# Optimization experiments

Hardware: AMD Instinct MI355X
Metric: run time of the kernel (lower is better)

Reference implementation:

```python
import jax, jax.numpy as jnp
import numpy as np

H = 512; EMB = 300; TAGE = 20; TRE = 20
VOCAB = 50000; NTAGS = 50; NTRANS = 100; NCONST = 80
B = 128; S = 256; T = 512; R = S // 2


def _lstm_scan(x, Wih, Whh, b):
    # x: [N, L, D] -> hidden states [N, L, H]; torch gate order i, f, g, o
    N = x.shape[0]; Hh = Whh.shape[1]
    xg = jnp.einsum('nld,gd->nlg', x, Wih) + b  # precompute input projections
    def step(carry, xg_t):
        h, c = carry
        g = xg_t + h @ Whh.T
        i, f, gg, o = jnp.split(g, 4, axis=-1)
        c = jax.nn.sigmoid(f) * c + jax.nn.sigmoid(i) * jnp.tanh(gg)
        h = jax.nn.sigmoid(o) * jnp.tanh(c)
        return (h, c), h
    h0 = jnp.zeros((N, Hh), x.dtype)
    _, hs = jax.lax.scan(step, (h0, h0), jnp.swapaxes(xg, 0, 1))
    return jnp.swapaxes(hs, 0, 1)


def setup_inputs() -> dict:
    key = jax.random.key(0)
    ks = iter(jax.random.split(key, 40))
    def p(shape, scale):
        return jax.random.normal(next(ks), shape, jnp.float32) * jnp.float32(scale)
    def lstm_p(din):
        s = 1.0 / np.sqrt(H)
        return p((4 * H, din), s), p((4 * H, H), s), p((4 * H,), s)
    inp = {}
    inp['word_idx'] = jax.random.randint(next(ks), (B, S), 0, VOCAB)
    inp['tag_idx'] = jax.random.randint(next(ks), (B, S), 0, NTAGS)
    inp['transition_idx'] = jax.random.randint(next(ks), (B, T), 0, NTRANS)
    inp['label_idx'] = jax.random.randint(next(ks), (B, R), 0, NCONST)
    inp['emb'] = p((VOCAB, EMB), 1.0)
    inp['tag_emb'] = p((NTAGS, TAGE), 1.0)
    inp['tr_emb'] = p((NTRANS, TRE), 1.0)
    inp['const_emb'] = p((NCONST, H), 1.0)
    inp['word_Wih'], inp['word_Whh'], inp['word_b'] = lstm_p(EMB + TAGE)
    inp['tr_Wih'], inp['tr_Whh'], inp['tr_b'] = lstm_p(TRE)
    inp['con_Wih'], inp['con_Whh'], inp['con_b'] = lstm_p(H)
    inp['fwd_Wih'], inp['fwd_Whh'], inp['fwd_b'] = lstm_p(H)
    inp['bwd_Wih'], inp['bwd_Whh'], inp['bwd_b'] = lstm_p(H)
    inp['w2c_W'] = p((H, H), 1.0 / np.sqrt(H)); inp['w2c_b'] = jnp.zeros((H,), jnp.float32)
    inp['red_W'] = p((H, 2 * H), 1.0 / np.sqrt(2 * H)); inp['red_b'] = jnp.zeros((H,), jnp.float32)
    inp['out_W'] = p((NTRANS, 3 * H), 1.0 / np.sqrt(3 * H)); inp['out_b'] = jnp.zeros((NTRANS,), jnp.float32)
    return inp


def reference(word_idx, tag_idx, transition_idx, label_idx, emb, tag_emb, tr_emb, const_emb, word_Wih, word_Whh, word_b, tr_Wih, tr_Whh, tr_b, con_Wih, con_Whh, con_b, fwd_Wih, fwd_Whh, fwd_b, bwd_Wih, bwd_Whh, bwd_b, w2c_W, w2c_b, red_W, red_b, out_W, out_b):
    Bn, Sn = word_idx.shape
    Rn = label_idx.shape[1]
    # initial_word_queue: word emb + tag emb -> word LSTM
    word_in = jnp.concatenate([emb[word_idx], tag_emb[tag_idx]], axis=-1)  # [B,S,EMB+TAGE]
    word_h = _lstm_scan(word_in, word_Wih, word_Whh, word_b)              # [B,S,H]
    # transform_word_to_constituent
    c0 = word_h @ w2c_W.T + w2c_b                                         # [B,S,H]
    # build_constituent: label emb + 2 children through fwd/bwd reduce LSTMs
    lab = const_emb[label_idx]                                            # [B,R,H]
    ch0 = c0[:, 0::2][:, :Rn]; ch1 = c0[:, 1::2][:, :Rn]
    fwd_seq = jnp.stack([lab, ch0, ch1], axis=2).reshape(Bn * Rn, 3, -1)
    bwd_seq = jnp.stack([lab, ch1, ch0], axis=2).reshape(Bn * Rn, 3, -1)
    fh = _lstm_scan(fwd_seq, fwd_Wih, fwd_Whh, fwd_b)[:, -1]
    bh = _lstm_scan(bwd_seq, bwd_Wih, bwd_Whh, bwd_b)[:, -1]
    red = jnp.tanh(jnp.concatenate([fh, bh], -1) @ red_W.T + red_b).reshape(Bn, Rn, -1)
    # push_constituent: constituent LSTMCell scan over built constituents
    const_h = _lstm_scan(red, con_Wih, con_Whh, con_b)[:, -1]             # [B,H]
    # push_transition: transition LSTMCell scan
    tr_h = _lstm_scan(tr_emb[transition_idx], tr_Wih, tr_Whh, tr_b)[:, -1]  # [B,H]
    # forward(): W over concat(word_hx, transition_hx, constituent_hx)
    hx = jnp.concatenate([word_h[:, -1], tr_h, const_h], axis=-1)         # [B,3H]
    return hx @ out_W.T + out_b                                           # [B,NTRANS]
```

## Files before the change

### kernel.cpp

```cpp
#include <hip/hip_runtime.h>

typedef unsigned short u16;
typedef unsigned int u32;
typedef unsigned long long u64;
typedef __attribute__((ext_vector_type(8))) short short8;
typedef __attribute__((ext_vector_type(4))) float f32x4;

namespace {
constexpr int kS  = 256;
constexpr int kT  = 512;
constexpr int kNT = 100;
constexpr int LDST = 40;
}

__device__ __forceinline__ float bf(u16 v){ return __uint_as_float(((u32)v)<<16); }
__device__ __forceinline__ u16 f2bf(float f){
  u32 u = __float_as_uint(f);
  return (u16)((u + 0x7fffu + ((u>>16)&1u)) >> 16);
}
__device__ __forceinline__ float sigm(float x){ return 1.f/(1.f+__expf(-x)); }
__device__ __forceinline__ float tanha(float x){ return 2.f/(1.f+__expf(-2.f*x)) - 1.f; }
__device__ __forceinline__ float wred(float v){
  #pragma unroll
  for (int off=32; off>0; off>>=1) v += __shfl_xor(v, off, 64);
  return v;
}

__device__ __forceinline__ u64 ld_sys_u64(const void* p){
  return __hip_atomic_load((const u64*)p, __ATOMIC_RELAXED, __HIP_MEMORY_SCOPE_SYSTEM);
}
__device__ __forceinline__ void st_sys_u32(void* p, u32 v){
  __hip_atomic_store((u32*)p, v, __ATOMIC_RELAXED, __HIP_MEMORY_SCOPE_SYSTEM);
}
__device__ __forceinline__ u32 ld_sys_u32(const void* p){
  return __hip_atomic_load((const u32*)p, __ATOMIC_RELAXED, __HIP_MEMORY_SCOPE_SYSTEM);
}

__global__ void k_zero(u32* p, int n){
  const int i = blockIdx.x*256 + threadIdx.x;
  if (i < n) p[i] = 0;
}

struct SeqJob {
  u16* hseq; u16* hb0; u16* hb1;
  const u16* xg; const int* idx;
  float* c_io;
  const u16* Bw;
  u32* flags;
  int s_begin, s_end, mode, c_store;
};

__global__ __launch_bounds__(256,1) void k_seq2(SeqJob jA, SeqJob jB)
{
  __shared__ u16 Bs[32*520];
  __shared__ float c_lds[128*9];
  __shared__ float sc[4*4*16*20];
  const SeqJob j = (blockIdx.x < 64) ? jA : jB;
  const int gb = blockIdx.x & 63;
  const int tid = threadIdx.x;
  const int ln = tid & 63, w = tid >> 6, wm = w * 32;
  const int fr = ln & 15, koff = (ln >> 4) * 8;
  const int n0 = gb * 32, jh0 = gb * 8;

  for (int e = tid; e < 2048; e += 256) {
    const int cl = e >> 6, kb = (e & 63) * 8;
    *(uint4*)&Bs[cl*520 + kb] = *(const uint4*)&j.Bw[(size_t)(n0+cl)*512 + kb];
  }
  for (int e = tid; e < 1024; e += 256) {
    const int m = e >> 3, jj = e & 7;
    c_lds[m*9 + jj] = j.c_io[(size_t)m*512 + jh0 + jj];
  }
  __syncthreads();

  const size_t aoff0 = (size_t)(wm + fr)*512 + koff;
  const size_t aoff1 = (size_t)(wm + 16 + fr)*512 + koff;
  const int cr = (ln>>4)*4, cc = ln&15;
  const int trow = ln>>2, pp = ln&3, ntp = pp>>1, cp = pp&1;
  const f32x4 z4 = {0.f,0.f,0.f,0.f};

  for (int s = j.s_begin; s < j.s_end; ++s) {
    const u16* Ab; u16* hout;
    if (j.mode == 0) { Ab = j.hseq + (size_t)(s-1)*65536; hout = j.hseq + (size_t)s*65536; }
    else { Ab = ((s-1)&1) ? j.hb1 : j.hb0; hout = (s&1) ? j.hb1 : j.hb0; }
    const u16* xgs = (j.mode == 0) ? (j.xg + (size_t)s*262144) : j.xg;

    u64 aq0[16][2], aq1[16][2];
    #pragma unroll
    for (int kt = 0; kt < 16; ++kt) {
      aq0[kt][0] = ld_sys_u64(&Ab[aoff0 + kt*32]);
      aq0[kt][1] = ld_sys_u64(&Ab[aoff0 + kt*32 + 4]);
      aq1[kt][0] = ld_sys_u64(&Ab[aoff1 + kt*32]);
      aq1[kt][1] = ld_sys_u64(&Ab[aoff1 + kt*32 + 4]);
    }
    f32x4 acc[2][2] = {{z4,z4},{z4,z4}};
    #pragma unroll
    for (int kt = 0; kt < 16; ++kt) {
      union { u64 q[2]; short8 v; } ua, ub;
      ua.q[0] = aq0[kt][0]; ua.q[1] = aq0[kt][1];
      ub.q[0] = aq1[kt][0]; ub.q[1] = aq1[kt][1];
      const short8 b0 = *(const short8*)&Bs[fr*520 + kt*32 + koff];
      const short8 b1 = *(const short8*)&Bs[(16+fr)*520 + kt*32 + koff];
      acc[0][0] = __builtin_amdgcn_mfma_f32_16x16x32_bf16(ua.v, b0, acc[0][0], 0,0,0);
      acc[0][1] = __builtin_amdgcn_mfma_f32_16x16x32_bf16(ua.v, b1, acc[0][1], 0,0,0);
      acc[1][0] = __builtin_amdgcn_mfma_f32_16x16x32_bf16(ub.v, b0, acc[1][0], 0,0,0);
      acc[1][1] = __builtin_amdgcn_mfma_f32_16x16x32_bf16(ub.v, b1, acc[1][1], 0,0,0);
    }

    #pragma unroll
    for (int mt=0; mt<2; ++mt)
      #pragma unroll
      for (int nt=0; nt<2; ++nt) {
        float* scb = &sc[(size_t)(w*4 + mt*2 + nt)*320];
        #pragma unroll
        for (int ri=0; ri<4; ++ri) scb[(cr+ri)*20 + cc] = acc[mt][nt][ri];
      }
    #pragma unroll
    for (int mt=0; mt<2; ++mt) {
      const int m = wm + mt*16 + trow;
      const float* scb = &sc[(size_t)(w*4+mt*2+ntp)*320 + trow*20 + cp*8];
      const float4 zlo = *(const float4*)&scb[0];
      const float4 zhi = *(const float4*)&scb[4];
      long xr;
      if (j.mode == 0) xr = m;
      else if (j.mode == 1) xr = j.idx[(size_t)m*512 + s];
      else xr = (long)m*128 + s;
      union { uint4 u4; u16 h[8]; } xq;
      xq.u4 = *(const uint4*)&xgs[(size_t)xr*2048 + n0 + ntp*16 + cp*8];
      const int cj = m*9 + ntp*4 + cp*2;
      float h0, h1;
      {
        const float i_ = sigm(zlo.x + bf(xq.h[0]));
        const float f_ = sigm(zlo.y + bf(xq.h[1]));
        const float g_ = tanha(zlo.z + bf(xq.h[2]));
        const float o_ = sigm(zlo.w + bf(xq.h[3]));
        const float cn = f_*c_lds[cj] + i_*g_;
        c_lds[cj] = cn;
        h0 = o_*tanha(cn);
      }
      {
        const float i_ = sigm(zhi.x + bf(xq.h[4]));
        const float f_ = sigm(zhi.y + bf(xq.h[5]));
        const float g_ = tanha(zhi.z + bf(xq.h[6]));
        const float o_ = sigm(zhi.w + bf(xq.h[7]));
        const float cn = f_*c_lds[cj+1] + i_*g_;
        c_lds[cj+1] = cn;
        h1 = o_*tanha(cn);
      }
      const u32 pk = (u32)f2bf(h0) | ((u32)f2bf(h1) << 16);
      st_sys_u32(&hout[(size_t)m*512 + jh0 + ntp*4 + cp*2], pk);
    }

    __builtin_amdgcn_s_waitcnt(0);
    __syncthreads();
    if (tid == 0)
      st_sys_u32(j.flags + (gb << 5), (u32)s);
    if (s + 1 < j.s_end) {
      if (tid < 64) {
        while (true) {
          u32 f = ld_sys_u32(j.flags + (tid << 5));
          if (__all((int)(f >= (u32)s))) break;
          __builtin_amdgcn_s_sleep(2);
        }
      }
      __syncthreads();
    }
  }
  if (j.c_store) {
    __syncthreads();
    for (int e = tid; e < 1024; e += 256) {
      const int m = e >> 3, jj = e & 7;
      j.c_io[(size_t)m*512 + jh0 + jj] = c_lds[m*9 + jj];
    }
  }
}

__device__ __forceinline__ void gemm_core(
    const u16* __restrict__ A, const u16* __restrict__ B, int K,
    int m0, int n0, u16* As, u16* Bs, f32x4 acc[4][4], int tid)
{
  const int lane = tid & 63;
  const int w = tid >> 6;
  const int wm = (w & 1) * 64, wn = (w >> 1) * 64;
  const int fr = lane & 15;
  const int fq = (lane >> 4) * 8;
  for (int k0 = 0; k0 < K; k0 += 32) {
    __syncthreads();
    #pragma unroll
    for (int it = 0; it < 2; ++it) {
      const int l = tid + it * 256;
      const int r = l >> 2, kq = (l & 3) * 8;
      *(uint4*)&As[r * LDST + kq] = *(const uint4*)&A[(size_t)(m0 + r) * K + k0 + kq];
      *(uint4*)&Bs[r * LDST + kq] = *(const uint4*)&B[(size_t)(n0 + r) * K + k0 + kq];
    }
    __syncthreads();
    short8 af[4], bfr[4];
    #pragma unroll
    for (int t = 0; t < 4; ++t) {
      af[t]  = *(const short8*)&As[(wm + t * 16 + fr) * LDST + fq];
      bfr[t] = *(const short8*)&Bs[(wn + t * 16 + fr) * LDST + fq];
    }
    #pragma unroll
    for (int mt = 0; mt < 4; ++mt)
      #pragma unroll
      for (int nt = 0; nt < 4; ++nt)
        acc[mt][nt] = __builtin_amdgcn_mfma_f32_16x16x32_bf16(af[mt], bfr[nt], acc[mt][nt], 0, 0, 0);
  }
}

__global__ __launch_bounds__(256) void k_gemm(
    const u16* __restrict__ A, const u16* __restrict__ B, u16* __restrict__ C,
    const float* __restrict__ bias, int K, int N, int tanh_flag)
{
  __shared__ u16 As[128 * LDST];
  __shared__ u16 Bs[128 * LDST];
  const int tid = threadIdx.x;
  const int m0 = blockIdx.x * 128, n0 = blockIdx.y * 128;
  f32x4 acc[4][4];
  const f32x4 z4 = {0.f, 0.f, 0.f, 0.f};
  #pragma unroll
  for (int mt = 0; mt < 4; ++mt)
    #pragma unroll
    for (int nt = 0; nt < 4; ++nt) acc[mt][nt] = z4;

  gemm_core(A, B, K, m0, n0, As, Bs, acc, tid);

  const int lane = tid & 63;
  const int w = tid >> 6;
  const int wm = (w & 1) * 64, wn = (w >> 1) * 64;
  const int cr = (lane >> 4) * 4, cc = lane & 15;
  #pragma unroll
  for (int mt = 0; mt < 4; ++mt)
    #pragma unroll
    for (int nt = 0; nt < 4; ++nt)
      #pragma unroll
      for (int ri = 0; ri < 4; ++ri) {
        const int row = m0 + wm + mt * 16 + cr + ri;
        const int col = n0 + wn + nt * 16 + cc;
        float v = acc[mt][nt][ri];
        if (bias) v += bias[col];
        if (tanh_flag) v = tanha(v);
        C[(size_t)row * N + col] = f2bf(v);
      }
}

__global__ __launch_bounds__(256) void k_lstm_cat(
    const u16* __restrict__ H, const u16* __restrict__ X,
    const u16* __restrict__ B, const float* __restrict__ bias,
    const int* __restrict__ idx, int cmode, int p0, int first,
    float* __restrict__ c_st, u16* __restrict__ h_out, int h_stride, int h_coloff)
{
  __shared__ u16 As[128 * LDST];
  __shared__ u16 Bs[128 * LDST];
  __shared__ float zb[64 * 128];
  const int tid = threadIdx.x;
  const int m0 = blockIdx.x * 128, n0 = blockIdx.y * 128;
  const int lane = tid & 63;
  const int w = tid >> 6;
  const int wm = (w & 1) * 64, wn = (w >> 1) * 64;
  const int fr = lane & 15, fq = (lane >> 4) * 8;
  f32x4 acc[4][4];
  const f32x4 z4 = {0.f, 0.f, 0.f, 0.f};
  #pragma unroll
  for (int mt = 0; mt < 4; ++mt)
    #pragma unroll
    for (int nt = 0; nt < 4; ++nt) acc[mt][nt] = z4;

  for (int k0 = first ? 512 : 0; k0 < 1024; k0 += 32) {
    __syncthreads();
    #pragma unroll
    for (int it = 0; it < 2; ++it) {
      const int l = tid + it * 256;
      const int r = l >> 2, kq = (l & 3) * 8;
      const int m = m0 + r;
      const u16* src;
      if (k0 < 512) {
        src = H + (size_t)m * 512 + k0 + kq;
      } else {
        long xr;
        if (cmode == 1)      xr = (long)(2 * (m & 127) + p0) * 128 + (m >> 7);
        else if (cmode == 2) xr = (long)idx[m];
        else                 xr = (long)m * 128 + p0;
        src = X + (size_t)xr * 512 + (k0 - 512) + kq;
      }
      *(uint4*)&As[r * LDST + kq] = *(const uint4*)src;
      *(uint4*)&Bs[r * LDST + kq] = *(const uint4*)&B[(size_t)(n0 + r) * 1024 + k0 + kq];
    }
    __syncthreads();
    short8 af[4], bfr[4];
    #pragma unroll
    for (int t = 0; t < 4; ++t) {
      af[t]  = *(const short8*)&As[(wm + t * 16 + fr) * LDST + fq];
      bfr[t] = *(const short8*)&Bs[(wn + t * 16 + fr) * LDST + fq];
    }
    #pragma unroll
    for (int mt = 0; mt < 4; ++mt)
      #pragma unroll
      for (int nt = 0; nt < 4; ++nt)
        acc[mt][nt] = __builtin_amdgcn_mfma_f32_16x16x32_bf16(af[mt], bfr[nt], acc[mt][nt], 0, 0, 0);
  }

  const int cr = (lane >> 4) * 4, cc = lane & 15;
  #pragma unroll
  for (int half = 0; half < 2; ++half) {
    __syncthreads();
    if (wm == half * 64) {
      #pragma unroll
      for (int mt = 0; mt < 4; ++mt)
        #pragma unroll
        for (int nt = 0; nt < 4; ++nt)
          #pragma unroll
          for (int ri = 0; ri < 4; ++ri)
            zb[(mt * 16 + cr + ri) * 128 + wn + nt * 16 + cc] = acc[mt][nt][ri];
    }
    __syncthreads();
    for (int c = tid; c < 2048; c += 256) {
      const int rl = c >> 5;
      const int q  = c & 31;
      const int m  = m0 + half * 64 + rl;
      const int jh = (n0 >> 2) + q;
      const float4 bv = *(const float4*)&bias[n0 + q * 4];
      const float4 zv = *(const float4*)&zb[rl * 128 + q * 4];
      const float i_ = sigm(zv.x + bv.x);
      const float f_ = sigm(zv.y + bv.y);
      const float g_ = tanha(zv.z + bv.z);
      const float o_ = sigm(zv.w + bv.w);
      const size_t ci = (size_t)m * 512 + jh;
      const float cold = first ? 0.f : c_st[ci];
      const float cn = f_ * cold + i_ * g_;
      c_st[ci] = cn;
      h_out[(size_t)m * h_stride + h_coloff + jh] = f2bf(o_ * tanha(cn));
    }
  }
}

__global__ __launch_bounds__(256) void k_gate0(
    const u16* __restrict__ xg, int xg_mode, int p0,
    const int* __restrict__ idx, int istride,
    float* __restrict__ c_st, u16* __restrict__ h_out, int h_stride, int h_coloff, int M)
{
  const int id = blockIdx.x * 256 + threadIdx.x;
  if (id >= M * 512) return;
  const int m = id >> 9, jh = id & 511;
  long xr;
  if (xg_mode == 0) xr = (long)m * p0;
  else              xr = (long)idx[(size_t)m * istride];
  const ushort4 xq = *(const ushort4*)&xg[(size_t)xr * 2048 + jh * 4];
  const float i_ = sigm(bf(xq.x));
  const float g_ = tanha(bf(xq.z));
  const float o_ = sigm(bf(xq.w));
  const float cn = i_ * g_;
  c_st[(size_t)m * 512 + jh] = cn;
  h_out[(size_t)m * h_stride + h_coloff + jh] = f2bf(o_ * tanha(cn));
}

__global__ void k_perm_w(const float* __restrict__ in, u16* __restrict__ out,
                         int Ksrc, int Kfill, int Ktot, int coff)
{
  const int rp = blockIdx.x;
  const int g = rp & 3, jh = rp >> 2;
  const float* src = in + (size_t)(g * 512 + jh) * Ksrc;
  for (int k = threadIdx.x; k < Kfill; k += 256)
    out[(size_t)rp * Ktot + coff + k] = f2bf(k < Ksrc ? src[k] : 0.f);
}
__global__ void k_perm_b(const float* __restrict__ in, float* __restrict__ out)
{
  const int rp = blockIdx.x * 256 + threadIdx.x;
  out[rp] = in[(rp & 3) * 512 + (rp >> 2)];
}
__global__ void k_cvt(const float* __restrict__ in, u16* __restrict__ out, int n)
{
  const int i = blockIdx.x * 256 + threadIdx.x;
  if (i < n) out[i] = f2bf(in[i]);
}
__global__ void k_pad2d(const float* __restrict__ in, u16* __restrict__ out,
                        int Rin, int Kin, int Kout)
{
  const int r = blockIdx.x;
  for (int k = threadIdx.x; k < Kout; k += 256)
    out[(size_t)r * Kout + k] = f2bf((r < Rin && k < Kin) ? in[(size_t)r * Kin + k] : 0.f);
}
__global__ void k_gather_word(const int* __restrict__ widx, const int* __restrict__ tidx,
                              const float* __restrict__ emb, const float* __restrict__ temb,
                              u16* __restrict__ Aw)
{
  const int row = blockIdx.x;
  const int s = row >> 7, b = row & 127;
  const int wi = widx[b * kS + s];
  const int ti = tidx[b * kS + s];
  for (int t = threadIdx.x; t < 320; t += 256)
    Aw[(size_t)row * 320 + t] = f2bf(t < 300 ? emb[(size_t)wi * 300 + t] : temb[ti * 20 + t - 300]);
}

__global__ __launch_bounds__(256) void k_out(
    const u16* __restrict__ wh, const u16* __restrict__ trh, const u16* __restrict__ conh,
    const float* __restrict__ W, const float* __restrict__ bias, float* __restrict__ out)
{
  const int wid = blockIdx.x * 4 + (threadIdx.x >> 6);
  const int lane = threadIdx.x & 63;
  const int b = wid / kNT;
  const int t = wid - b * kNT;
  const u16* s0 = wh + (size_t)b * 512;
  const u16* s1 = trh + (size_t)b * 512;
  const u16* s2 = conh + (size_t)b * 512;
  const float* wr = W + (size_t)t * 1536;
  float acc = 0.f;
  #pragma unroll
  for (int i = 0; i < 8; ++i) acc += bf(s0[i * 64 + lane]) * wr[i * 64 + lane];
  #pragma unroll
  for (int i = 0; i < 8; ++i) acc += bf(s1[i * 64 + lane]) * wr[512 + i * 64 + lane];
  #pragma unroll
  for (int i = 0; i < 8; ++i) acc += bf(s2[i * 64 + lane]) * wr[1024 + i * 64 + lane];
  acc = wred(acc);
  if (lane == 0) out[(size_t)b * kNT + t] = acc + bias[t];
}

extern "C" void kernel_launch(void* const* d_in, const int* in_sizes, int n_in,
                              void* d_out, int out_size, void* d_ws, size_t ws_size,
                              hipStream_t stream)
{
  (void)in_sizes; (void)n_in; (void)out_size; (void)ws_size;
  const int* word_idx = (const int*)d_in[0];
  const int* tag_idx  = (const int*)d_in[1];
  const int* tr_idx   = (const int*)d_in[2];
  const int* lab_idx  = (const int*)d_in[3];
  const float* emb       = (const float*)d_in[4];
  const float* tag_emb   = (const float*)d_in[5];
  const float* tr_emb    = (const float*)d_in[6];
  const float* const_emb = (const float*)d_in[7];
  const float* word_Wih = (const float*)d_in[8];
  const float* word_Whh = (const float*)d_in[9];
  const float* word_b   = (const float*)d_in[10];
  const float* tr_Wih = (const float*)d_in[11];
  const float* tr_Whh = (const float*)d_in[12];
  const float* tr_b   = (const float*)d_in[13];
  const float* con_Wih = (const float*)d_in[14];
  const float* con_Whh = (const float*)d_in[15];
  const float* con_b   = (const float*)d_in[16];
  const float* fwd_Wih = (const float*)d_in[17];
  const float* fwd_Whh = (const float*)d_in[18];
  const float* fwd_b   = (const float*)d_in[19];
  const float* bwd_Wih = (const float*)d_in[20];
  const float* bwd_Whh = (const float*)d_in[21];
  const float* bwd_b   = (const float*)d_in[22];
  const float* w2c_W = (const float*)d_in[23];
  const float* w2c_b = (const float*)d_in[24];
  const float* red_W = (const float*)d_in[25];
  const float* red_b = (const float*)d_in[26];
  const float* out_W = (const float*)d_in[27];
  const float* out_b = (const float*)d_in[28];

  char* p = (char*)d_ws;
  auto alloc = [&](size_t bytes)->void* {
    void* r = (void*)p; p += (bytes + 255) & ~(size_t)255; return r;
  };
  u16* word_h = (u16*)alloc((size_t)32768*512*2);
  char* R     = (char*)alloc((size_t)155189248);
  u16* A_word = (u16*)(R);
  u16* XGword = (u16*)(R + 20971520);
  u16* c0     = (u16*)(R);
  u16* h1     = (u16*)(R + 33554432);
  u16* h2     = (u16*)(R + 50331648);
  float* c_big= (float*)(R + 67108864);
  u16* fb     = (u16*)(R + 100663296);
  u16* red    = (u16*)(R + 134217728);
  u16* XG_con = (u16*)(R);
  u16* wWih = (u16*)alloc((size_t)2048*320*2);
  u16* wWhh = (u16*)alloc((size_t)2048*512*2);
  u16* tWih = (u16*)alloc((size_t)2048*32*2);
  u16* tWhh = (u16*)alloc((size_t)2048*512*2);
  u16* cWihp = (u16*)alloc((size_t)2048*512*2);
  u16* cWhhp = (u16*)alloc((size_t)2048*512*2);
  u16* fWcat = (u16*)alloc((size_t)2048*1024*2);
  u16* bWcat = (u16*)alloc((size_t)2048*1024*2);
  u16* fWih  = (u16*)alloc((size_t)2048*512*2);
  u16* bWih  = (u16*)alloc((size_t)2048*512*2);
  u16* w2cWb = (u16*)alloc((size_t)512*512*2);
  u16* redWb = (u16*)alloc((size_t)512*1024*2);
  u16* A80   = (u16*)alloc((size_t)128*512*2);
  u16* Atr   = (u16*)alloc((size_t)128*32*2);
  u16* tbltr = (u16*)alloc((size_t)128*2048*2);
  u16* tbl0  = (u16*)alloc((size_t)128*2048*2);
  float* b_word = (float*)alloc(2048*4);
  float* b_tr   = (float*)alloc(2048*4);
  float* b_con  = (float*)alloc(2048*4);
  float* b_fwd  = (float*)alloc(2048*4);
  float* b_bwd  = (float*)alloc(2048*4);
  float* c_word = (float*)alloc((size_t)128*512*4);
  float* c_tr   = (float*)alloc((size_t)128*512*4);
  float* c_con  = (float*)alloc((size_t)128*512*4);
  u16* trh1 = (u16*)alloc((size_t)128*512*2);
  u16* trh2 = (u16*)alloc((size_t)128*512*2);
  u16* ch1  = (u16*)alloc((size_t)128*512*2);
  u16* ch2  = (u16*)alloc((size_t)128*512*2);
  u32* flags = (u32*)alloc((size_t)4*64*32*4);

  k_zero<<<32,256,0,stream>>>(flags, 4*64*32);

  k_perm_w<<<2048,256,0,stream>>>(word_Wih, wWih, 320, 320, 320, 0);
  k_perm_w<<<2048,256,0,stream>>>(word_Whh, wWhh, 512, 512, 512, 0);
  k_perm_w<<<2048,256,0,stream>>>(tr_Wih,   tWih, 20,  32,  32,  0);
  k_perm_w<<<2048,256,0,stream>>>(tr_Whh,   tWhh, 512, 512, 512, 0);
  k_perm_w<<<2048,256,0,stream>>>(con_Wih,  cWihp, 512, 512, 512, 0);
  k_perm_w<<<2048,256,0,stream>>>(con_Whh,  cWhhp, 512, 512, 512, 0);
  k_perm_w<<<2048,256,0,stream>>>(fwd_Whh,  fWcat, 512, 512, 1024, 0);
  k_perm_w<<<2048,256,0,stream>>>(fwd_Wih,  fWcat, 512, 512, 1024, 512);
  k_perm_w<<<2048,256,0,stream>>>(bwd_Whh,  bWcat, 512, 512, 1024, 0);
  k_perm_w<<<2048,256,0,stream>>>(bwd_Wih,  bWcat, 512, 512, 1024, 512);
  k_perm_w<<<2048,256,0,stream>>>(fwd_Wih,  fWih, 512, 512, 512, 0);
  k_perm_w<<<2048,256,0,stream>>>(bwd_Wih,  bWih, 512, 512, 512, 0);
  k_perm_b<<<8,256,0,stream>>>(word_b, b_word);
  k_perm_b<<<8,256,0,stream>>>(tr_b,   b_tr);
  k_perm_b<<<8,256,0,stream>>>(con_b,  b_con);
  k_perm_b<<<8,256,0,stream>>>(fwd_b,  b_fwd);
  k_perm_b<<<8,256,0,stream>>>(bwd_b,  b_bwd);
  k_cvt<<<1024,256,0,stream>>>(w2c_W, w2cWb, 512*512);
  k_cvt<<<2048,256,0,stream>>>(red_W, redWb, 512*1024);
  k_pad2d<<<128,256,0,stream>>>(const_emb, A80, 80, 512, 512);
  k_pad2d<<<128,256,0,stream>>>(tr_emb,    Atr, 100, 20, 32);
  k_gather_word<<<32768,256,0,stream>>>(word_idx, tag_idx, emb, tag_emb, A_word);

  k_gemm<<<dim3(256,16),256,0,stream>>>(A_word, wWih, XGword, b_word, 320, 2048, 0);
  k_gemm<<<dim3(1,16),256,0,stream>>>(Atr, tWih, tbltr, b_tr, 32, 2048, 0);

  k_gate0<<<256,256,0,stream>>>(XGword, 0, 1, nullptr, 0, c_word, word_h, 512, 0, 128);
  k_gate0<<<256,256,0,stream>>>(tbltr, 2, 0, tr_idx, 512, c_tr, trh1, 512, 0, 128);

  SeqJob jw{ word_h, nullptr, nullptr, XGword, nullptr, c_word, wWhh, flags + 0*2048, 1, 256, 0, 0 };
  SeqJob jt1{ nullptr, trh1, trh2, tbltr, tr_idx, c_tr, tWhh, flags + 1*2048, 1, 256, 1, 1 };
  k_seq2<<<128,256,0,stream>>>(jw, jt1);

  k_gemm<<<dim3(256,4),256,0,stream>>>(word_h, w2cWb, c0, w2c_b, 512, 512, 0);

  k_gemm<<<dim3(1,16),256,0,stream>>>(A80, fWih, tbl0, b_fwd, 512, 2048, 0);
  k_gate0<<<32768,256,0,stream>>>(tbl0, 2, 0, lab_idx, 1, c_big, h1, 512, 0, 16384);
  k_lstm_cat<<<dim3(128,16),256,0,stream>>>(h1, c0, fWcat, b_fwd, nullptr, 1, 0, 0, c_big, h2, 512, 0);
  k_lstm_cat<<<dim3(128,16),256,0,stream>>>(h2, c0, fWcat, b_fwd, nullptr, 1, 1, 0, c_big, fb, 1024, 0);
  k_gemm<<<dim3(1,16),256,0,stream>>>(A80, bWih, tbl0, b_bwd, 512, 2048, 0);
  k_gate0<<<32768,256,0,stream>>>(tbl0, 2, 0, lab_idx, 1, c_big, h1, 512, 0, 16384);
  k_lstm_cat<<<dim3(128,16),256,0,stream>>>(h1, c0, bWcat, b_bwd, nullptr, 1, 1, 0, c_big, h2, 512, 0);
  k_lstm_cat<<<dim3(128,16),256,0,stream>>>(h2, c0, bWcat, b_bwd, nullptr, 1, 0, 0, c_big, fb, 1024, 512);

  k_gemm<<<dim3(128,4),256,0,stream>>>(fb, redWb, red, red_b, 1024, 512, 1);

  k_gemm<<<dim3(128,16),256,0,stream>>>(red, cWihp, XG_con, b_con, 512, 2048, 0);

  k_gate0<<<256,256,0,stream>>>(XG_con, 0, 128, nullptr, 0, c_con, ch1, 512, 0, 128);

  SeqJob jc{ nullptr, ch1, ch2, XG_con, nullptr, c_con, cWhhp, flags + 2*2048, 1, 128, 2, 0 };
  SeqJob jt2{ nullptr, trh1, trh2, tbltr, tr_idx, c_tr, tWhh, flags + 3*2048, 256, 512, 1, 0 };
  k_seq2<<<128,256,0,stream>>>(jc, jt2);

  k_out<<<3200,256,0,stream>>>(word_h + (size_t)255*128*512, trh2, ch2,
                               out_W, out_b, (float*)d_out);
}
```

Before: 6.398 ms.

## Use ring-buffered hidden-state sequences so recurrent loads are plain vector loads

```diff
diff --git a/kernel.cpp b/kernel.cpp
--- a/kernel.cpp
+++ b/kernel.cpp
@@ -26,9 +26,6 @@
   return v;
 }
 
-__device__ __forceinline__ u64 ld_sys_u64(const void* p){
-  return __hip_atomic_load((const u64*)p, __ATOMIC_RELAXED, __HIP_MEMORY_SCOPE_SYSTEM);
-}
 __device__ __forceinline__ void st_sys_u32(void* p, u32 v){
   __hip_atomic_store((u32*)p, v, __ATOMIC_RELAXED, __HIP_MEMORY_SCOPE_SYSTEM);
 }
@@ -42,7 +39,7 @@
 }
 
 struct SeqJob {
-  u16* hseq; u16* hb0; u16* hb1;
+  u16* hseq;
   const u16* xg; const int* idx;
   float* c_io;
   const u16* Bw;
@@ -79,25 +76,35 @@
   const f32x4 z4 = {0.f,0.f,0.f,0.f};
 
   for (int s = j.s_begin; s < j.s_end; ++s) {
-    const u16* Ab; u16* hout;
-    if (j.mode == 0) { Ab = j.hseq + (size_t)(s-1)*65536; hout = j.hseq + (size_t)s*65536; }
-    else { Ab = ((s-1)&1) ? j.hb1 : j.hb0; hout = (s&1) ? j.hb1 : j.hb0; }
+    const u16* Ab = j.hseq + (size_t)((s-1)&255)*65536;
+    u16* hout     = j.hseq + (size_t)(s&255)*65536;
     const u16* xgs = (j.mode == 0) ? (j.xg + (size_t)s*262144) : j.xg;
 
-    u64 aq0[16][2], aq1[16][2];
+    int xrow[2];
+    #pragma unroll
+    for (int mt = 0; mt < 2; ++mt) {
+      const int m = wm + mt*16 + trow;
+      if (j.mode == 1)      xrow[mt] = j.idx[(size_t)m*512 + s];
+      else if (j.mode == 0) xrow[mt] = m;
+      else                  xrow[mt] = m*128 + s;
+    }
+
+    uint4 aq0[16], aq1[16];
     #pragma unroll
     for (int kt = 0; kt < 16; ++kt) {
-      aq0[kt][0] = ld_sys_u64(&Ab[aoff0 + kt*32]);
-      aq0[kt][1] = ld_sys_u64(&Ab[aoff0 + kt*32 + 4]);
-      aq1[kt][0] = ld_sys_u64(&Ab[aoff1 + kt*32]);
-      aq1[kt][1] = ld_sys_u64(&Ab[aoff1 + kt*32 + 4]);
-    }
+      aq0[kt] = *(const uint4*)&Ab[aoff0 + kt*32];
+      aq1[kt] = *(const uint4*)&Ab[aoff1 + kt*32];
+    }
+    uint4 xqv[2];
+    #pragma unroll
+    for (int mt = 0; mt < 2; ++mt)
+      xqv[mt] = *(const uint4*)&xgs[(size_t)xrow[mt]*2048 + n0 + ntp*16 + cp*8];
+
     f32x4 acc[2][2] = {{z4,z4},{z4,z4}};
     #pragma unroll
     for (int kt = 0; kt < 16; ++kt) {
-      union { u64 q[2]; short8 v; } ua, ub;
-      ua.q[0] = aq0[kt][0]; ua.q[1] = aq0[kt][1];
-      ub.q[0] = aq1[kt][0]; ub.q[1] = aq1[kt][1];
+      union { uint4 q; short8 v; } ua, ub;
+      ua.q = aq0[kt]; ub.q = aq1[kt];
       const short8 b0 = *(const short8*)&Bs[fr*520 + kt*32 + koff];
       const short8 b1 = *(const short8*)&Bs[(16+fr)*520 + kt*32 + koff];
       acc[0][0] = __builtin_amdgcn_mfma_f32_16x16x32_bf16(ua.v, b0, acc[0][0], 0,0,0);
@@ -120,12 +127,8 @@
       const float* scb = &sc[(size_t)(w*4+mt*2+ntp)*320 + trow*20 + cp*8];
       const float4 zlo = *(const float4*)&scb[0];
       const float4 zhi = *(const float4*)&scb[4];
-      long xr;
-      if (j.mode == 0) xr = m;
-      else if (j.mode == 1) xr = j.idx[(size_t)m*512 + s];
-      else xr = (long)m*128 + s;
       union { uint4 u4; u16 h[8]; } xq;
-      xq.u4 = *(const uint4*)&xgs[(size_t)xr*2048 + n0 + ntp*16 + cp*8];
+      xq.u4 = xqv[mt];
       const int cj = m*9 + ntp*4 + cp*2;
       float h0, h1;
       {
@@ -153,13 +156,13 @@
     __builtin_amdgcn_s_waitcnt(0);
     __syncthreads();
     if (tid == 0)
-      st_sys_u32(j.flags + (gb << 5), (u32)s);
+      st_sys_u32(j.flags + gb, (u32)s);
     if (s + 1 < j.s_end) {
       if (tid < 64) {
         while (true) {
-          u32 f = ld_sys_u32(j.flags + (tid << 5));
+          u32 f = ld_sys_u32(j.flags + tid);
           if (__all((int)(f >= (u32)s))) break;
-          __builtin_amdgcn_s_sleep(2);
+          __builtin_amdgcn_s_sleep(1);
         }
       }
       __syncthreads();
@@ -453,17 +456,19 @@
   auto alloc = [&](size_t bytes)->void* {
     void* r = (void*)p; p += (bytes + 255) & ~(size_t)255; return r;
   };
-  u16* word_h = (u16*)alloc((size_t)32768*512*2);
-  char* R     = (char*)alloc((size_t)155189248);
+  u16* word_h = (u16*)alloc((size_t)33554432);
+  char* R     = (char*)alloc((size_t)167772160);
   u16* A_word = (u16*)(R);
-  u16* XGword = (u16*)(R + 20971520);
-  u16* c0     = (u16*)(R);
-  u16* h1     = (u16*)(R + 33554432);
-  u16* h2     = (u16*)(R + 50331648);
-  float* c_big= (float*)(R + 67108864);
-  u16* fb     = (u16*)(R + 100663296);
-  u16* red    = (u16*)(R + 134217728);
-  u16* XG_con = (u16*)(R);
+  u16* XGword = (u16*)(R + 33554432);
+  u16* trseq  = (u16*)(R);
+  u16* c0     = (u16*)(R + 33554432);
+  u16* h1     = (u16*)(R + 67108864);
+  u16* h2     = (u16*)(R + 83886080);
+  float* c_big= (float*)(R + 100663296);
+  u16* fb     = (u16*)(R + 134217728);
+  u16* red    = (u16*)(R);
+  u16* XG_con = (u16*)(R + 67108864);
+  u16* conseq = (u16*)(R + 134217728);
   u16* wWih = (u16*)alloc((size_t)2048*320*2);
   u16* wWhh = (u16*)alloc((size_t)2048*512*2);
   u16* tWih = (u16*)alloc((size_t)2048*32*2);
@@ -488,13 +493,9 @@
   float* c_word = (float*)alloc((size_t)128*512*4);
   float* c_tr   = (float*)alloc((size_t)128*512*4);
   float* c_con  = (float*)alloc((size_t)128*512*4);
-  u16* trh1 = (u16*)alloc((size_t)128*512*2);
-  u16* trh2 = (u16*)alloc((size_t)128*512*2);
-  u16* ch1  = (u16*)alloc((size_t)128*512*2);
-  u16* ch2  = (u16*)alloc((size_t)128*512*2);
-  u32* flags = (u32*)alloc((size_t)4*64*32*4);
-
-  k_zero<<<32,256,0,stream>>>(flags, 4*64*32);
+  u32* flags = (u32*)alloc((size_t)4*64*4);
+
+  k_zero<<<1,256,0,stream>>>(flags, 4*64);
 
   k_perm_w<<<2048,256,0,stream>>>(word_Wih, wWih, 320, 320, 320, 0);
   k_perm_w<<<2048,256,0,stream>>>(word_Whh, wWhh, 512, 512, 512, 0);
@@ -523,10 +524,10 @@
   k_gemm<<<dim3(1,16),256,0,stream>>>(Atr, tWih, tbltr, b_tr, 32, 2048, 0);
 
   k_gate0<<<256,256,0,stream>>>(XGword, 0, 1, nullptr, 0, c_word, word_h, 512, 0, 128);
-  k_gate0<<<256,256,0,stream>>>(tbltr, 2, 0, tr_idx, 512, c_tr, trh1, 512, 0, 128);
-
-  SeqJob jw{ word_h, nullptr, nullptr, XGword, nullptr, c_word, wWhh, flags + 0*2048, 1, 256, 0, 0 };
-  SeqJob jt1{ nullptr, trh1, trh2, tbltr, tr_idx, c_tr, tWhh, flags + 1*2048, 1, 256, 1, 1 };
+  k_gate0<<<256,256,0,stream>>>(tbltr, 2, 0, tr_idx, 512, c_tr, trseq, 512, 0, 128);
+
+  SeqJob jw { word_h, XGword, nullptr, c_word, wWhh, flags + 0*64, 1, 256, 0, 0 };
+  SeqJob jt1{ trseq,  tbltr,  tr_idx,  c_tr,   tWhh, flags + 1*64, 1, 256, 1, 1 };
   k_seq2<<<128,256,0,stream>>>(jw, jt1);
 
   k_gemm<<<dim3(256,4),256,0,stream>>>(word_h, w2cWb, c0, w2c_b, 512, 512, 0);
@@ -544,12 +545,12 @@
 
   k_gemm<<<dim3(128,16),256,0,stream>>>(red, cWihp, XG_con, b_con, 512, 2048, 0);
 
-  k_gate0<<<256,256,0,stream>>>(XG_con, 0, 128, nullptr, 0, c_con, ch1, 512, 0, 128);
-
-  SeqJob jc{ nullptr, ch1, ch2, XG_con, nullptr, c_con, cWhhp, flags + 2*2048, 1, 128, 2, 0 };
-  SeqJob jt2{ nullptr, trh1, trh2, tbltr, tr_idx, c_tr, tWhh, flags + 3*2048, 256, 512, 1, 0 };
+  k_gate0<<<256,256,0,stream>>>(XG_con, 0, 128, nullptr, 0, c_con, conseq, 512, 0, 128);
+
+  SeqJob jc { conseq, XG_con, nullptr, c_con, cWhhp, flags + 2*64, 1,   128, 2, 0 };
+  SeqJob jt2{ trseq,  tbltr,  tr_idx,  c_tr,  tWhh,  flags + 3*64, 256, 512, 1, 0 };
   k_seq2<<<128,256,0,stream>>>(jc, jt2);
 
-  k_out<<<3200,256,0,stream>>>(word_h + (size_t)255*128*512, trh2, ch2,
-                               out_W, out_b, (float*)d_out);
-}
+  k_out<<<3200,256,0,stream>>>(word_h + (size_t)255*65536, trseq + (size_t)255*65536,
+                               conseq + (size_t)127*65536, out_W, out_b, (float*)d_out);
+}
```

After: 5.241 ms. -18.1%, faster.
